# Performance work log

Hardware: AMD Instinct MI355X
Metric: run time of the kernel (lower is better)

Reference implementation:

```python
import jax, jax.numpy as jnp
import numpy as np

TOP_K = 2

def setup_inputs() -> dict:
    key = jax.random.key(0)
    ks = jax.random.split(key, 5)
    B, T, D, F, E = 4, 2048, 1024, 4096, 8
    s = 0.02
    return {
        "x": jax.random.normal(ks[0], (B, T, D), jnp.float32),
        "gate_w": jax.random.normal(ks[1], (D, E), jnp.float32) * s,
        "w1": jax.random.normal(ks[2], (E, D, F), jnp.float32) * s,
        "w3": jax.random.normal(ks[3], (E, D, F), jnp.float32) * s,
        "w2": jax.random.normal(ks[4], (E, F, D), jnp.float32) * s,
    }

def reference(x, gate_w, w1, w3, w2):
    # Router: logits -> softmax -> top-k -> renormalize (eval mode: no jitter)
    logits = jnp.einsum("btd,de->bte", x, gate_w)          # (B,T,E)
    probs = jax.nn.softmax(logits, axis=-1)
    expert_weights, expert_indices = jax.lax.top_k(probs, TOP_K)  # (B,T,K)
    expert_weights = expert_weights / expert_weights.sum(-1, keepdims=True)

    E = w1.shape[0]
    out = jnp.zeros_like(x)
    # Loop over small fixed expert count; per-token weight is 0 for non-routed
    # tokens, so dense compute + weighted sum matches the masked gather/scatter.
    for i in range(E):
        wi = jnp.where(expert_indices == i, expert_weights, 0.0).sum(-1)  # (B,T)
        h = jax.nn.silu(jnp.einsum("btd,df->btf", x, w1[i])) \
            * jnp.einsum("btd,df->btf", x, w3[i])                         # SwiGLU
        out = out + jnp.einsum("btf,fd->btd", h, w2[i]) * wi[..., None]
    return out
```

## Files before the change

### kernel.cpp

```cpp
#include <hip/hip_runtime.h>
#include <hip/hip_bf16.h>


#define NTOK 8192
#define DMODEL 1024
#define FDIM 4096
#define NEXP 8

typedef __attribute__((ext_vector_type(8))) short s8v;
typedef __attribute__((ext_vector_type(4))) float f4v;

__device__ __forceinline__ int imin(int a, int b){ return a < b ? a : b; }

__device__ __forceinline__ unsigned short f2b(float f){
  union { float f; unsigned u; } v; v.f = f;
  unsigned r = v.u + 0x7fffu + ((v.u >> 16) & 1u);
  return (unsigned short)(r >> 16);
}

__device__ __forceinline__ f4v mfma16(s8v a, s8v b, f4v c){
  return __builtin_amdgcn_mfma_f32_16x16x32_bf16(a, b, c, 0, 0, 0);
}

#define GLDS16(gp, lp) __builtin_amdgcn_global_load_lds(                      \
    (const __attribute__((address_space(1))) void*)(gp),                      \
    (__attribute__((address_space(3))) void*)(lp), 16, 0, 0)


__global__ void k_cvt(const float4* __restrict__ in, ushort4* __restrict__ out, int n4){
  int i = blockIdx.x * blockDim.x + threadIdx.x;
  int st = gridDim.x * blockDim.x;
  for(; i < n4; i += st){
    float4 v = in[i];
    ushort4 o;
    o.x = f2b(v.x); o.y = f2b(v.y); o.z = f2b(v.z); o.w = f2b(v.w);
    out[i] = o;
  }
}

__global__ void k_tr(const float* __restrict__ in, unsigned short* __restrict__ out,
                     int R, int C){
  __shared__ float tile[32][33];
  const float* src = in + (size_t)blockIdx.z * R * C;
  unsigned short* dst = out + (size_t)blockIdx.z * R * C;
  int bx = blockIdx.x * 32, by = blockIdx.y * 32;
  int tx = threadIdx.x & 31, ty = threadIdx.x >> 5;
  #pragma unroll
  for(int i = 0; i < 32; i += 8)
    tile[ty + i][tx] = src[(size_t)(by + ty + i) * C + bx + tx];
  __syncthreads();
  #pragma unroll
  for(int i = 0; i < 32; i += 8)
    dst[(size_t)(bx + ty + i) * R + by + tx] = f2b(tile[tx][ty + i]);
}

__global__ void k_router(const float* __restrict__ x, const float* __restrict__ gw,
                         int* __restrict__ route_e, float* __restrict__ route_w,
                         int* __restrict__ counts){
  int lane = threadIdx.x & 63;
  int t = blockIdx.x * 4 + (threadIdx.x >> 6);
  const float* xr = x + (size_t)t * DMODEL;
  float acc[NEXP];
  #pragma unroll
  for(int e = 0; e < NEXP; e++) acc[e] = 0.f;
  for(int d = lane; d < DMODEL; d += 64){
    float xv = xr[d];
    const float* g = gw + d * NEXP;
    #pragma unroll
    for(int e = 0; e < NEXP; e++) acc[e] += xv * g[e];
  }
  #pragma unroll
  for(int off = 32; off > 0; off >>= 1){
    #pragma unroll
    for(int e = 0; e < NEXP; e++) acc[e] += __shfl_down(acc[e], off, 64);
  }
  if(lane == 0){
    float mx = acc[0];
    #pragma unroll
    for(int e = 1; e < NEXP; e++) mx = fmaxf(mx, acc[e]);
    float p[NEXP];
    #pragma unroll
    for(int e = 0; e < NEXP; e++) p[e] = expf(acc[e] - mx);
    int i0 = 0;
    #pragma unroll
    for(int e = 1; e < NEXP; e++) if(p[e] > p[i0]) i0 = e;
    int i1 = (i0 == 0) ? 1 : 0;
    #pragma unroll
    for(int e = 0; e < NEXP; e++) if(e != i0 && p[e] > p[i1]) i1 = e;
    float inv = 1.f / (p[i0] + p[i1]);
    route_e[2*t]   = i0; route_e[2*t+1] = i1;
    route_w[2*t]   = p[i0] * inv;
    route_w[2*t+1] = p[i1] * inv;
    atomicAdd(&counts[i0], 1); atomicAdd(&counts[i1], 1);
  }
}

__global__ void k_scan(const int* __restrict__ counts, int* __restrict__ offsets,
                       int* __restrict__ cursor){
  if(threadIdx.x == 0){
    int o = 0;
    for(int e = 0; e < NEXP; e++){ offsets[e] = o; o += counts[e]; cursor[e] = 0; }
    offsets[NEXP] = o;
  }
}

__global__ void k_fill(const int* __restrict__ route_e, const float* __restrict__ route_w,
                       const int* __restrict__ offsets, int* __restrict__ cursor,
                       int* __restrict__ pair_tok, float* __restrict__ pair_wt,
                       int* __restrict__ t2p){
  int t = blockIdx.x * blockDim.x + threadIdx.x;
  if(t >= NTOK) return;
  #pragma unroll
  for(int k = 0; k < 2; k++){
    int e = route_e[2*t + k];
    int pos = atomicAdd(&cursor[e], 1);
    int gidx = offsets[e] + pos;
    pair_tok[gidx] = t;
    pair_wt[gidx] = route_w[2*t + k];
    t2p[2*t + k] = gidx;
  }
}

__global__ __launch_bounds__(256, 2) void k_ffn1(
    const unsigned short* __restrict__ xb,
    const unsigned short* __restrict__ w1t,
    const unsigned short* __restrict__ w3t,
    const int* __restrict__ counts, const int* __restrict__ offsets,
    const int* __restrict__ pair_tok,
    unsigned short* __restrict__ h)
{
  int e = blockIdx.z;
  int cnt = counts[e];
  int m0 = blockIdx.x * 128;
  if(m0 >= cnt) return;
  int off = offsets[e];
  int n0 = blockIdx.y * 128;

  __shared__ short As[2][128*32];
  __shared__ short B1s[2][128*32];
  __shared__ short B3s[2][128*32];
  __shared__ int stok[128];

  int tid = threadIdx.x;
  if(tid < 128){
    int pr = m0 + tid;
    stok[tid] = pair_tok[off + imin(pr, cnt - 1)];
  }
  __syncthreads();

  int wave = tid >> 6, lane = tid & 63;
  int rr  = wave * 32 + (lane >> 2);
  int g16 = (((lane & 3) ^ ((lane >> 3) & 3))) * 16;
  int wo = wave * 32 * 32;

  const char* a0 = (const char*)xb + (size_t)stok[rr]      * (DMODEL*2) + g16;
  const char* a1 = (const char*)xb + (size_t)stok[rr + 16] * (DMODEL*2) + g16;
  const char* b1base = (const char*)w1t + ((size_t)e * FDIM + n0) * (DMODEL*2);
  const char* b3base = (const char*)w3t + ((size_t)e * FDIM + n0) * (DMODEL*2);
  const char* b1_0 = b1base + (size_t)rr * (DMODEL*2) + g16;
  const char* b1_1 = b1_0 + (size_t)16 * (DMODEL*2);
  const char* b3_0 = b3base + (size_t)rr * (DMODEL*2) + g16;
  const char* b3_1 = b3_0 + (size_t)16 * (DMODEL*2);

  f4v zero = {0.f, 0.f, 0.f, 0.f};
  f4v acc1[4][4], acc3[4][4];
  #pragma unroll
  for(int i = 0; i < 4; i++)
    #pragma unroll
    for(int j = 0; j < 4; j++){ acc1[i][j] = zero; acc3[i][j] = zero; }

  int wm = wave & 1, wn = wave >> 1;
  int lm = lane & 15, quad = lane >> 4;
  int rp = (quad ^ ((lm >> 1) & 3)) * 8;

  GLDS16(a0,   As[0]  + wo); GLDS16(a1,   As[0]  + wo + 512);
  GLDS16(b1_0, B1s[0] + wo); GLDS16(b1_1, B1s[0] + wo + 512);
  GLDS16(b3_0, B3s[0] + wo); GLDS16(b3_1, B3s[0] + wo + 512);
  __syncthreads();

  for(int kt = 0; kt < DMODEL; kt += 32){
    int c = (kt >> 5) & 1;
    if(kt + 32 < DMODEL){
      int kb = (kt + 32) * 2;
      short* an  = As[c^1]  + wo;
      short* b1n = B1s[c^1] + wo;
      short* b3n = B3s[c^1] + wo;
      GLDS16(a0   + kb, an);  GLDS16(a1   + kb, an  + 512);
      GLDS16(b1_0 + kb, b1n); GLDS16(b1_1 + kb, b1n + 512);
      GLDS16(b3_0 + kb, b3n); GLDS16(b3_1 + kb, b3n + 512);
    }

    const short* Ab  = As[c];
    const short* B1b = B1s[c];
    const short* B3b = B3s[c];
    s8v af[4], b1f[4], b3f[4];
    #pragma unroll
    for(int mi = 0; mi < 4; mi++)
      af[mi] = *(const s8v*)(Ab + (wm*64 + mi*16 + lm)*32 + rp);
    #pragma unroll
    for(int ni = 0; ni < 4; ni++){
      b1f[ni] = *(const s8v*)(B1b + (wn*64 + ni*16 + lm)*32 + rp);
      b3f[ni] = *(const s8v*)(B3b + (wn*64 + ni*16 + lm)*32 + rp);
    }
    #pragma unroll
    for(int mi = 0; mi < 4; mi++)
      #pragma unroll
      for(int ni = 0; ni < 4; ni++){
        acc1[mi][ni] = mfma16(af[mi], b1f[ni], acc1[mi][ni]);
        acc3[mi][ni] = mfma16(af[mi], b3f[ni], acc3[mi][ni]);
      }
    __syncthreads();
  }

  #pragma unroll
  for(int mi = 0; mi < 4; mi++){
    int prb = m0 + wm*64 + mi*16 + quad*4;
    #pragma unroll
    for(int i = 0; i < 4; i++){
      int pr = prb + i;
      if(pr < cnt){
        size_t hrow = (size_t)(off + pr) * FDIM + n0 + wn*64 + lm;
        #pragma unroll
        for(int ni = 0; ni < 4; ni++){
          float p = acc1[mi][ni][i];
          float q = acc3[mi][ni][i];
          float hv = (p / (1.f + __expf(-p))) * q;
          h[hrow + ni*16] = f2b(hv);
        }
      }
    }
  }
}

__global__ __launch_bounds__(256, 2) void k_ffn2(
    const unsigned short* __restrict__ h,
    const unsigned short* __restrict__ w2t,
    const int* __restrict__ counts, const int* __restrict__ offsets,
    const float* __restrict__ pair_wt,
    float* __restrict__ pout)
{
  int e = blockIdx.z;
  int cnt = counts[e];
  int m0 = blockIdx.x * 128;
  if(m0 >= cnt) return;
  int off = offsets[e];
  int n0 = blockIdx.y * 128;

  __shared__ short As[2][128*32];
  __shared__ short Bs[2][128*32];

  int tid = threadIdx.x, wave = tid >> 6, lane = tid & 63;
  int rr  = wave * 32 + (lane >> 2);
  int g16 = (((lane & 3) ^ ((lane >> 3) & 3))) * 16;
  int wo = wave * 32 * 32;

  int pr0 = imin(m0 + rr,      cnt - 1);
  int pr1 = imin(m0 + rr + 16, cnt - 1);
  const char* a0 = (const char*)h + (size_t)(off + pr0) * (FDIM*2) + g16;
  const char* a1 = (const char*)h + (size_t)(off + pr1) * (FDIM*2) + g16;
  const char* bbase = (const char*)w2t + ((size_t)e * DMODEL + n0) * (FDIM*2);
  const char* b0 = bbase + (size_t)rr * (FDIM*2) + g16;
  const char* b1p = b0 + (size_t)16 * (FDIM*2);

  f4v zero = {0.f, 0.f, 0.f, 0.f};
  f4v acc[4][4];
  #pragma unroll
  for(int i = 0; i < 4; i++)
    #pragma unroll
    for(int j = 0; j < 4; j++) acc[i][j] = zero;

  int wm = wave & 1, wn = wave >> 1;
  int lm = lane & 15, quad = lane >> 4;
  int rp = (quad ^ ((lm >> 1) & 3)) * 8;

  GLDS16(a0, As[0] + wo); GLDS16(a1,  As[0] + wo + 512);
  GLDS16(b0, Bs[0] + wo); GLDS16(b1p, Bs[0] + wo + 512);
  __syncthreads();

  for(int kt = 0; kt < FDIM; kt += 32){
    int c = (kt >> 5) & 1;
    if(kt + 32 < FDIM){
      int kb = (kt + 32) * 2;
      short* an = As[c^1] + wo;
      short* bn = Bs[c^1] + wo;
      GLDS16(a0  + kb, an); GLDS16(a1  + kb, an + 512);
      GLDS16(b0  + kb, bn); GLDS16(b1p + kb, bn + 512);
    }

    const short* Ab = As[c];
    const short* Bb = Bs[c];
    s8v af[4], bf[4];
    #pragma unroll
    for(int mi = 0; mi < 4; mi++)
      af[mi] = *(const s8v*)(Ab + (wm*64 + mi*16 + lm)*32 + rp);
    #pragma unroll
    for(int ni = 0; ni < 4; ni++)
      bf[ni] = *(const s8v*)(Bb + (wn*64 + ni*16 + lm)*32 + rp);
    #pragma unroll
    for(int mi = 0; mi < 4; mi++)
      #pragma unroll
      for(int ni = 0; ni < 4; ni++)
        acc[mi][ni] = mfma16(af[mi], bf[ni], acc[mi][ni]);
    __syncthreads();
  }

  #pragma unroll
  for(int mi = 0; mi < 4; mi++){
    int prb = m0 + wm*64 + mi*16 + quad*4;
    #pragma unroll
    for(int i = 0; i < 4; i++){
      int pr = prb + i;
      if(pr < cnt){
        int gp = off + pr;
        float wt = pair_wt[gp];
        float* prow = pout + (size_t)gp * DMODEL + n0 + wn*64 + lm;
        #pragma unroll
        for(int ni = 0; ni < 4; ni++)
          prow[ni*16] = acc[mi][ni][i] * wt;
      }
    }
  }
}

__global__ void k_combine(const float4* __restrict__ pout, const int* __restrict__ t2p,
                          float4* __restrict__ out){
  int t = blockIdx.x;
  int d = threadIdx.x;
  int p0 = t2p[2*t], p1 = t2p[2*t + 1];
  out[(size_t)t * 256 + d] = pout[(size_t)p0 * 256 + d] + pout[(size_t)p1 * 256 + d];
}

extern "C" void kernel_launch(void* const* d_in, const int* in_sizes, int n_in,
                              void* d_out, int out_size, void* d_ws, size_t ws_size,
                              hipStream_t stream){
  const float* x  = (const float*)d_in[0];
  const float* gw = (const float*)d_in[1];
  const float* w1 = (const float*)d_in[2];
  const float* w3 = (const float*)d_in[3];
  const float* w2 = (const float*)d_in[4];
  float* out = (float*)d_out;

  char* ws = (char*)d_ws;
  size_t o = 0;
  auto alloc = [&](size_t b){ size_t r = o; o += (b + 255) & ~(size_t)255; return r; };
  unsigned short* xb  = (unsigned short*)(ws + alloc((size_t)NTOK * DMODEL * 2));
  unsigned short* w1t = (unsigned short*)(ws + alloc((size_t)NEXP * DMODEL * FDIM * 2));
  unsigned short* w3t = (unsigned short*)(ws + alloc((size_t)NEXP * DMODEL * FDIM * 2));
  unsigned short* w2t = (unsigned short*)(ws + alloc((size_t)NEXP * DMODEL * FDIM * 2));
  unsigned short* h   = (unsigned short*)(ws + alloc((size_t)2 * NTOK * FDIM * 2));
  int*   route_e  = (int*)  (ws + alloc(2 * NTOK * 4));
  float* route_w  = (float*)(ws + alloc(2 * NTOK * 4));
  int*   counts   = (int*)  (ws + alloc(256));
  int*   offsets  = (int*)  (ws + alloc(256));
  int*   cursor   = (int*)  (ws + alloc(256));
  int*   pair_tok = (int*)  (ws + alloc(2 * NTOK * 4));
  float* pair_wt  = (float*)(ws + alloc(2 * NTOK * 4));
  int*   t2p      = (int*)  (ws + alloc(2 * NTOK * 4));
  float* pout = (float*)w1t;

  hipMemsetAsync(counts, 0, 256, stream);

  k_cvt<<<2048, 256, 0, stream>>>((const float4*)x, (ushort4*)xb, NTOK * DMODEL / 4);
  k_tr<<<dim3(FDIM/32, DMODEL/32, NEXP), 256, 0, stream>>>(w1, w1t, DMODEL, FDIM);
  k_tr<<<dim3(FDIM/32, DMODEL/32, NEXP), 256, 0, stream>>>(w3, w3t, DMODEL, FDIM);
  k_tr<<<dim3(DMODEL/32, FDIM/32, NEXP), 256, 0, stream>>>(w2, w2t, FDIM, DMODEL);

  k_router<<<NTOK/4, 256, 0, stream>>>(x, gw, route_e, route_w, counts);
  k_scan<<<1, 64, 0, stream>>>(counts, offsets, cursor);
  k_fill<<<NTOK/256, 256, 0, stream>>>(route_e, route_w, offsets, cursor, pair_tok, pair_wt, t2p);

  k_ffn1<<<dim3(64, FDIM/128, NEXP), 256, 0, stream>>>(xb, w1t, w3t, counts, offsets, pair_tok, h);
  k_ffn2<<<dim3(64, DMODEL/128, NEXP), 256, 0, stream>>>(h, w2t, counts, offsets, pair_wt, pout);
  k_combine<<<NTOK, 256, 0, stream>>>((const float4*)pout, t2p, (float4*)out);
}
```

Before: 1.630 ms.

## Restructure grouped GEMMs with 512-thread tiles, split-phase pipelining and block swizzle

```diff
diff --git a/kernel.cpp b/kernel.cpp
--- a/kernel.cpp
+++ b/kernel.cpp
@@ -6,9 +6,12 @@
 #define DMODEL 1024
 #define FDIM 4096
 #define NEXP 8
+#define NT1 (DMODEL/64)
+#define NT2 (FDIM/64)
 
 typedef __attribute__((ext_vector_type(8))) short s8v;
 typedef __attribute__((ext_vector_type(4))) float f4v;
+typedef __attribute__((ext_vector_type(8))) unsigned short us8;
 
 __device__ __forceinline__ int imin(int a, int b){ return a < b ? a : b; }
 
@@ -25,6 +28,11 @@
 #define GLDS16(gp, lp) __builtin_amdgcn_global_load_lds(                      \
     (const __attribute__((address_space(1))) void*)(gp),                      \
     (__attribute__((address_space(3))) void*)(lp), 16, 0, 0)
+
+#define WAIT_LGK  asm volatile("s_waitcnt lgkmcnt(0)" ::: "memory")
+#define WAIT_V4   asm volatile("s_waitcnt vmcnt(4) lgkmcnt(0)" ::: "memory")
+#define WAIT_V0   asm volatile("s_waitcnt vmcnt(0) lgkmcnt(0)" ::: "memory")
+#define BAR       __builtin_amdgcn_s_barrier()
 
 
 __global__ void k_cvt(const float4* __restrict__ in, ushort4* __restrict__ out, int n4){
@@ -40,18 +48,28 @@
 
 __global__ void k_tr(const float* __restrict__ in, unsigned short* __restrict__ out,
                      int R, int C){
-  __shared__ float tile[32][33];
+  __shared__ float tile[64][65];
   const float* src = in + (size_t)blockIdx.z * R * C;
   unsigned short* dst = out + (size_t)blockIdx.z * R * C;
-  int bx = blockIdx.x * 32, by = blockIdx.y * 32;
-  int tx = threadIdx.x & 31, ty = threadIdx.x >> 5;
-  #pragma unroll
-  for(int i = 0; i < 32; i += 8)
-    tile[ty + i][tx] = src[(size_t)(by + ty + i) * C + bx + tx];
+  int bx = blockIdx.x * 64, by = blockIdx.y * 64;
+  int tid = threadIdx.x;
+  int tx = tid & 15, ty = tid >> 4;
+  #pragma unroll
+  for(int i = 0; i < 64; i += 16){
+    float4 v = *(const float4*)&src[(size_t)(by + ty + i) * C + bx + tx*4];
+    tile[ty + i][tx*4 + 0] = v.x; tile[ty + i][tx*4 + 1] = v.y;
+    tile[ty + i][tx*4 + 2] = v.z; tile[ty + i][tx*4 + 3] = v.w;
+  }
   __syncthreads();
-  #pragma unroll
-  for(int i = 0; i < 32; i += 8)
-    dst[(size_t)(bx + ty + i) * R + by + tx] = f2b(tile[tx][ty + i]);
+  int oc = tid & 7, orow = tid >> 3;
+  #pragma unroll
+  for(int i = 0; i < 64; i += 32){
+    int r = orow + i;
+    us8 o;
+    #pragma unroll
+    for(int j = 0; j < 8; j++) o[j] = f2b(tile[oc*8 + j][r]);
+    *(us8*)&dst[(size_t)(bx + r) * R + by + oc*8] = o;
+  }
 }
 
 __global__ void k_router(const float* __restrict__ x, const float* __restrict__ gw,
@@ -121,7 +139,7 @@
   }
 }
 
-__global__ __launch_bounds__(256, 2) void k_ffn1(
+__global__ __launch_bounds__(512, 2) void k_ffn1(
     const unsigned short* __restrict__ xb,
     const unsigned short* __restrict__ w1t,
     const unsigned short* __restrict__ w3t,
@@ -129,38 +147,48 @@
     const int* __restrict__ pair_tok,
     unsigned short* __restrict__ h)
 {
-  int e = blockIdx.z;
+  unsigned lin = blockIdx.x + ((blockIdx.y + (blockIdx.z << 5)) << 6);
+  unsigned swz = ((lin & 7u) << 11) | (lin >> 3);
+  int e  = swz >> 11;
+  int bx = swz & 63;
+  int by = (swz >> 6) & 31;
+
   int cnt = counts[e];
-  int m0 = blockIdx.x * 128;
+  int m0 = bx * 256;
   if(m0 >= cnt) return;
   int off = offsets[e];
-  int n0 = blockIdx.y * 128;
-
-  __shared__ short As[2][128*32];
-  __shared__ short B1s[2][128*32];
-  __shared__ short B3s[2][128*32];
-  __shared__ int stok[128];
+  int n0 = by * 128;
+
+  __shared__ short As[2][2][256][32];
+  __shared__ short B1s[2][2][128][32];
+  __shared__ short B3s[2][2][128][32];
+  __shared__ int stok[256];
 
   int tid = threadIdx.x;
-  if(tid < 128){
-    int pr = m0 + tid;
-    stok[tid] = pair_tok[off + imin(pr, cnt - 1)];
-  }
+  if(tid < 256) stok[tid] = pair_tok[off + imin(m0 + tid, cnt - 1)];
   __syncthreads();
 
-  int wave = tid >> 6, lane = tid & 63;
-  int rr  = wave * 32 + (lane >> 2);
-  int g16 = (((lane & 3) ^ ((lane >> 3) & 3))) * 16;
-  int wo = wave * 32 * 32;
-
-  const char* a0 = (const char*)xb + (size_t)stok[rr]      * (DMODEL*2) + g16;
-  const char* a1 = (const char*)xb + (size_t)stok[rr + 16] * (DMODEL*2) + g16;
-  const char* b1base = (const char*)w1t + ((size_t)e * FDIM + n0) * (DMODEL*2);
-  const char* b3base = (const char*)w3t + ((size_t)e * FDIM + n0) * (DMODEL*2);
-  const char* b1_0 = b1base + (size_t)rr * (DMODEL*2) + g16;
-  const char* b1_1 = b1_0 + (size_t)16 * (DMODEL*2);
-  const char* b3_0 = b3base + (size_t)rr * (DMODEL*2) + g16;
-  const char* b3_1 = b3_0 + (size_t)16 * (DMODEL*2);
+  int w = tid >> 6, lane = tid & 63;
+  int lr = lane >> 2, g = lane & 3;
+  int gs = (g ^ ((lr >> 1) & 3)) * 16;
+
+  int rA0 = w*32 + lr, rA1 = rA0 + 16;
+  int rB  = w*16 + lr;
+  const char* pA0 = (const char*)xb + (size_t)stok[rA0] * (DMODEL*2) + gs;
+  const char* pA1 = (const char*)xb + (size_t)stok[rA1] * (DMODEL*2) + gs;
+  const char* pB1 = (const char*)w1t + ((size_t)e*FDIM + n0 + rB) * (DMODEL*2) + gs;
+  const char* pB3 = (const char*)w3t + ((size_t)e*FDIM + n0 + rB) * (DMODEL*2) + gs;
+
+  auto stageA = [&](int kt, int kk, int buf){
+    int kb = kt*128 + kk*64;
+    GLDS16(pA0 + kb, &As[buf][kk][w*32][0]);
+    GLDS16(pA1 + kb, &As[buf][kk][w*32 + 16][0]);
+  };
+  auto stageB = [&](int kt, int kk, int buf){
+    int kb = kt*128 + kk*64;
+    GLDS16(pB1 + kb, &B1s[buf][kk][w*16][0]);
+    GLDS16(pB3 + kb, &B3s[buf][kk][w*16][0]);
+  };
 
   f4v zero = {0.f, 0.f, 0.f, 0.f};
   f4v acc1[4][4], acc3[4][4];
@@ -169,47 +197,92 @@
     #pragma unroll
     for(int j = 0; j < 4; j++){ acc1[i][j] = zero; acc3[i][j] = zero; }
 
-  int wm = wave & 1, wn = wave >> 1;
+  int wm = w & 3, wn = w >> 2;
   int lm = lane & 15, quad = lane >> 4;
   int rp = (quad ^ ((lm >> 1) & 3)) * 8;
 
-  GLDS16(a0,   As[0]  + wo); GLDS16(a1,   As[0]  + wo + 512);
-  GLDS16(b1_0, B1s[0] + wo); GLDS16(b1_1, B1s[0] + wo + 512);
-  GLDS16(b3_0, B3s[0] + wo); GLDS16(b3_1, B3s[0] + wo + 512);
-  __syncthreads();
-
-  for(int kt = 0; kt < DMODEL; kt += 32){
-    int c = (kt >> 5) & 1;
-    if(kt + 32 < DMODEL){
-      int kb = (kt + 32) * 2;
-      short* an  = As[c^1]  + wo;
-      short* b1n = B1s[c^1] + wo;
-      short* b3n = B3s[c^1] + wo;
-      GLDS16(a0   + kb, an);  GLDS16(a1   + kb, an  + 512);
-      GLDS16(b1_0 + kb, b1n); GLDS16(b1_1 + kb, b1n + 512);
-      GLDS16(b3_0 + kb, b3n); GLDS16(b3_1 + kb, b3n + 512);
-    }
-
-    const short* Ab  = As[c];
-    const short* B1b = B1s[c];
-    const short* B3b = B3s[c];
-    s8v af[4], b1f[4], b3f[4];
-    #pragma unroll
-    for(int mi = 0; mi < 4; mi++)
-      af[mi] = *(const s8v*)(Ab + (wm*64 + mi*16 + lm)*32 + rp);
-    #pragma unroll
-    for(int ni = 0; ni < 4; ni++){
-      b1f[ni] = *(const s8v*)(B1b + (wn*64 + ni*16 + lm)*32 + rp);
-      b3f[ni] = *(const s8v*)(B3b + (wn*64 + ni*16 + lm)*32 + rp);
-    }
-    #pragma unroll
-    for(int mi = 0; mi < 4; mi++)
+  stageA(0, 0, 0); stageB(0, 0, 0); stageA(0, 1, 0); stageB(0, 1, 0);
+  WAIT_V4; BAR;
+
+  s8v b1f[4], b3f[4];
+  for(int t = 0; t < NT1; ++t){
+    int buf = t & 1;
+    bool last = (t == NT1 - 1);
+
+    if(!last) stageA(t+1, 0, buf^1);
+    {
+      s8v a0 = *(const s8v*)&As[buf][0][wm*64 +  0 + lm][rp];
+      s8v a1 = *(const s8v*)&As[buf][0][wm*64 + 16 + lm][rp];
       #pragma unroll
       for(int ni = 0; ni < 4; ni++){
-        acc1[mi][ni] = mfma16(af[mi], b1f[ni], acc1[mi][ni]);
-        acc3[mi][ni] = mfma16(af[mi], b3f[ni], acc3[mi][ni]);
-      }
-    __syncthreads();
+        b1f[ni] = *(const s8v*)&B1s[buf][0][wn*64 + ni*16 + lm][rp];
+        b3f[ni] = *(const s8v*)&B3s[buf][0][wn*64 + ni*16 + lm][rp];
+      }
+      __builtin_amdgcn_s_setprio(1);
+      #pragma unroll
+      for(int ni = 0; ni < 4; ni++){
+        acc1[0][ni] = mfma16(a0, b1f[ni], acc1[0][ni]);
+        acc3[0][ni] = mfma16(a0, b3f[ni], acc3[0][ni]);
+        acc1[1][ni] = mfma16(a1, b1f[ni], acc1[1][ni]);
+        acc3[1][ni] = mfma16(a1, b3f[ni], acc3[1][ni]);
+      }
+      __builtin_amdgcn_s_setprio(0);
+    }
+    WAIT_LGK; BAR;
+
+    if(!last) stageB(t+1, 0, buf^1);
+    {
+      s8v a2 = *(const s8v*)&As[buf][0][wm*64 + 32 + lm][rp];
+      s8v a3 = *(const s8v*)&As[buf][0][wm*64 + 48 + lm][rp];
+      __builtin_amdgcn_s_setprio(1);
+      #pragma unroll
+      for(int ni = 0; ni < 4; ni++){
+        acc1[2][ni] = mfma16(a2, b1f[ni], acc1[2][ni]);
+        acc3[2][ni] = mfma16(a2, b3f[ni], acc3[2][ni]);
+        acc1[3][ni] = mfma16(a3, b1f[ni], acc1[3][ni]);
+        acc3[3][ni] = mfma16(a3, b3f[ni], acc3[3][ni]);
+      }
+      __builtin_amdgcn_s_setprio(0);
+    }
+    if(!last) WAIT_V4; else WAIT_V0;
+    BAR;
+
+    if(!last) stageA(t+1, 1, buf^1);
+    {
+      s8v a0 = *(const s8v*)&As[buf][1][wm*64 +  0 + lm][rp];
+      s8v a1 = *(const s8v*)&As[buf][1][wm*64 + 16 + lm][rp];
+      #pragma unroll
+      for(int ni = 0; ni < 4; ni++){
+        b1f[ni] = *(const s8v*)&B1s[buf][1][wn*64 + ni*16 + lm][rp];
+        b3f[ni] = *(const s8v*)&B3s[buf][1][wn*64 + ni*16 + lm][rp];
+      }
+      __builtin_amdgcn_s_setprio(1);
+      #pragma unroll
+      for(int ni = 0; ni < 4; ni++){
+        acc1[0][ni] = mfma16(a0, b1f[ni], acc1[0][ni]);
+        acc3[0][ni] = mfma16(a0, b3f[ni], acc3[0][ni]);
+        acc1[1][ni] = mfma16(a1, b1f[ni], acc1[1][ni]);
+        acc3[1][ni] = mfma16(a1, b3f[ni], acc3[1][ni]);
+      }
+      __builtin_amdgcn_s_setprio(0);
+    }
+    WAIT_LGK; BAR;
+
+    if(!last) stageB(t+1, 1, buf^1);
+    {
+      s8v a2 = *(const s8v*)&As[buf][1][wm*64 + 32 + lm][rp];
+      s8v a3 = *(const s8v*)&As[buf][1][wm*64 + 48 + lm][rp];
+      __builtin_amdgcn_s_setprio(1);
+      #pragma unroll
+      for(int ni = 0; ni < 4; ni++){
+        acc1[2][ni] = mfma16(a2, b1f[ni], acc1[2][ni]);
+        acc3[2][ni] = mfma16(a2, b3f[ni], acc3[2][ni]);
+        acc1[3][ni] = mfma16(a3, b1f[ni], acc1[3][ni]);
+        acc3[3][ni] = mfma16(a3, b3f[ni], acc3[3][ni]);
+      }
+      __builtin_amdgcn_s_setprio(0);
+    }
+    if(!last){ WAIT_V4; BAR; }
   }
 
   #pragma unroll
@@ -225,88 +298,151 @@
           float p = acc1[mi][ni][i];
           float q = acc3[mi][ni][i];
           float hv = (p / (1.f + __expf(-p))) * q;
-          h[hrow + ni*16] = f2b(hv);
+          __builtin_nontemporal_store((unsigned short)f2b(hv), &h[hrow + ni*16]);
         }
       }
     }
   }
 }
 
-__global__ __launch_bounds__(256, 2) void k_ffn2(
+__global__ __launch_bounds__(512, 2) void k_ffn2(
     const unsigned short* __restrict__ h,
     const unsigned short* __restrict__ w2t,
     const int* __restrict__ counts, const int* __restrict__ offsets,
     const float* __restrict__ pair_wt,
     float* __restrict__ pout)
 {
-  int e = blockIdx.z;
+  unsigned lin = blockIdx.x + ((blockIdx.y + (blockIdx.z << 2)) << 6);
+  unsigned swz = ((lin & 7u) << 8) | (lin >> 3);
+  int e  = swz >> 8;
+  int bx = swz & 63;
+  int by = (swz >> 6) & 3;
+
   int cnt = counts[e];
-  int m0 = blockIdx.x * 128;
+  int m0 = bx * 256;
   if(m0 >= cnt) return;
   int off = offsets[e];
-  int n0 = blockIdx.y * 128;
-
-  __shared__ short As[2][128*32];
-  __shared__ short Bs[2][128*32];
-
-  int tid = threadIdx.x, wave = tid >> 6, lane = tid & 63;
-  int rr  = wave * 32 + (lane >> 2);
-  int g16 = (((lane & 3) ^ ((lane >> 3) & 3))) * 16;
-  int wo = wave * 32 * 32;
-
-  int pr0 = imin(m0 + rr,      cnt - 1);
-  int pr1 = imin(m0 + rr + 16, cnt - 1);
-  const char* a0 = (const char*)h + (size_t)(off + pr0) * (FDIM*2) + g16;
-  const char* a1 = (const char*)h + (size_t)(off + pr1) * (FDIM*2) + g16;
-  const char* bbase = (const char*)w2t + ((size_t)e * DMODEL + n0) * (FDIM*2);
-  const char* b0 = bbase + (size_t)rr * (FDIM*2) + g16;
-  const char* b1p = b0 + (size_t)16 * (FDIM*2);
+  int n0 = by * 256;
+
+  __shared__ short As[2][2][256][32];
+  __shared__ short Bs[2][2][256][32];
+
+  int tid = threadIdx.x, w = tid >> 6, lane = tid & 63;
+  int lr = lane >> 2, g = lane & 3;
+  int gs = (g ^ ((lr >> 1) & 3)) * 16;
+
+  int rA0 = w*32 + lr, rA1 = rA0 + 16;
+  int pr0 = imin(m0 + rA0, cnt - 1), pr1 = imin(m0 + rA1, cnt - 1);
+  const char* pA0 = (const char*)h + (size_t)(off + pr0) * (FDIM*2) + gs;
+  const char* pA1 = (const char*)h + (size_t)(off + pr1) * (FDIM*2) + gs;
+  const char* pB0 = (const char*)w2t + ((size_t)e*DMODEL + n0 + rA0) * (FDIM*2) + gs;
+  const char* pB1 = (const char*)w2t + ((size_t)e*DMODEL + n0 + rA1) * (FDIM*2) + gs;
+
+  auto stageA = [&](int kt, int kk, int buf){
+    int kb = kt*128 + kk*64;
+    GLDS16(pA0 + kb, &As[buf][kk][w*32][0]);
+    GLDS16(pA1 + kb, &As[buf][kk][w*32 + 16][0]);
+  };
+  auto stageB = [&](int kt, int kk, int buf){
+    int kb = kt*128 + kk*64;
+    GLDS16(pB0 + kb, &Bs[buf][kk][w*32][0]);
+    GLDS16(pB1 + kb, &Bs[buf][kk][w*32 + 16][0]);
+  };
 
   f4v zero = {0.f, 0.f, 0.f, 0.f};
-  f4v acc[4][4];
-  #pragma unroll
-  for(int i = 0; i < 4; i++)
+  f4v acc[8][4];
+  #pragma unroll
+  for(int i = 0; i < 8; i++)
     #pragma unroll
     for(int j = 0; j < 4; j++) acc[i][j] = zero;
 
-  int wm = wave & 1, wn = wave >> 1;
+  int wm = w & 1, wn = w >> 1;
   int lm = lane & 15, quad = lane >> 4;
   int rp = (quad ^ ((lm >> 1) & 3)) * 8;
 
-  GLDS16(a0, As[0] + wo); GLDS16(a1,  As[0] + wo + 512);
-  GLDS16(b0, Bs[0] + wo); GLDS16(b1p, Bs[0] + wo + 512);
-  __syncthreads();
-
-  for(int kt = 0; kt < FDIM; kt += 32){
-    int c = (kt >> 5) & 1;
-    if(kt + 32 < FDIM){
-      int kb = (kt + 32) * 2;
-      short* an = As[c^1] + wo;
-      short* bn = Bs[c^1] + wo;
-      GLDS16(a0  + kb, an); GLDS16(a1  + kb, an + 512);
-      GLDS16(b0  + kb, bn); GLDS16(b1p + kb, bn + 512);
-    }
-
-    const short* Ab = As[c];
-    const short* Bb = Bs[c];
-    s8v af[4], bf[4];
-    #pragma unroll
-    for(int mi = 0; mi < 4; mi++)
-      af[mi] = *(const s8v*)(Ab + (wm*64 + mi*16 + lm)*32 + rp);
-    #pragma unroll
-    for(int ni = 0; ni < 4; ni++)
-      bf[ni] = *(const s8v*)(Bb + (wn*64 + ni*16 + lm)*32 + rp);
-    #pragma unroll
-    for(int mi = 0; mi < 4; mi++)
+  stageA(0, 0, 0); stageB(0, 0, 0); stageA(0, 1, 0); stageB(0, 1, 0);
+  WAIT_V4; BAR;
+
+  s8v bf[4];
+  for(int t = 0; t < NT2; ++t){
+    int buf = t & 1;
+    bool last = (t == NT2 - 1);
+
+    if(!last) stageA(t+1, 0, buf^1);
+    {
+      s8v af[4];
+      #pragma unroll
+      for(int mi = 0; mi < 4; mi++)
+        af[mi] = *(const s8v*)&As[buf][0][wm*128 + mi*16 + lm][rp];
       #pragma unroll
       for(int ni = 0; ni < 4; ni++)
-        acc[mi][ni] = mfma16(af[mi], bf[ni], acc[mi][ni]);
-    __syncthreads();
-  }
-
-  #pragma unroll
-  for(int mi = 0; mi < 4; mi++){
-    int prb = m0 + wm*64 + mi*16 + quad*4;
+        bf[ni] = *(const s8v*)&Bs[buf][0][wn*64 + ni*16 + lm][rp];
+      __builtin_amdgcn_s_setprio(1);
+      #pragma unroll
+      for(int mi = 0; mi < 4; mi++)
+        #pragma unroll
+        for(int ni = 0; ni < 4; ni++)
+          acc[mi][ni] = mfma16(af[mi], bf[ni], acc[mi][ni]);
+      __builtin_amdgcn_s_setprio(0);
+    }
+    WAIT_LGK; BAR;
+
+    if(!last) stageB(t+1, 0, buf^1);
+    {
+      s8v af[4];
+      #pragma unroll
+      for(int mi = 0; mi < 4; mi++)
+        af[mi] = *(const s8v*)&As[buf][0][wm*128 + (4+mi)*16 + lm][rp];
+      __builtin_amdgcn_s_setprio(1);
+      #pragma unroll
+      for(int mi = 0; mi < 4; mi++)
+        #pragma unroll
+        for(int ni = 0; ni < 4; ni++)
+          acc[4+mi][ni] = mfma16(af[mi], bf[ni], acc[4+mi][ni]);
+      __builtin_amdgcn_s_setprio(0);
+    }
+    if(!last) WAIT_V4; else WAIT_V0;
+    BAR;
+
+    if(!last) stageA(t+1, 1, buf^1);
+    {
+      s8v af[4];
+      #pragma unroll
+      for(int mi = 0; mi < 4; mi++)
+        af[mi] = *(const s8v*)&As[buf][1][wm*128 + mi*16 + lm][rp];
+      #pragma unroll
+      for(int ni = 0; ni < 4; ni++)
+        bf[ni] = *(const s8v*)&Bs[buf][1][wn*64 + ni*16 + lm][rp];
+      __builtin_amdgcn_s_setprio(1);
+      #pragma unroll
+      for(int mi = 0; mi < 4; mi++)
+        #pragma unroll
+        for(int ni = 0; ni < 4; ni++)
+          acc[mi][ni] = mfma16(af[mi], bf[ni], acc[mi][ni]);
+      __builtin_amdgcn_s_setprio(0);
+    }
+    WAIT_LGK; BAR;
+
+    if(!last) stageB(t+1, 1, buf^1);
+    {
+      s8v af[4];
+      #pragma unroll
+      for(int mi = 0; mi < 4; mi++)
+        af[mi] = *(const s8v*)&As[buf][1][wm*128 + (4+mi)*16 + lm][rp];
+      __builtin_amdgcn_s_setprio(1);
+      #pragma unroll
+      for(int mi = 0; mi < 4; mi++)
+        #pragma unroll
+        for(int ni = 0; ni < 4; ni++)
+          acc[4+mi][ni] = mfma16(af[mi], bf[ni], acc[4+mi][ni]);
+      __builtin_amdgcn_s_setprio(0);
+    }
+    if(!last){ WAIT_V4; BAR; }
+  }
+
+  #pragma unroll
+  for(int mi = 0; mi < 8; mi++){
+    int prb = m0 + wm*128 + mi*16 + quad*4;
     #pragma unroll
     for(int i = 0; i < 4; i++){
       int pr = prb + i;
@@ -316,7 +452,7 @@
         float* prow = pout + (size_t)gp * DMODEL + n0 + wn*64 + lm;
         #pragma unroll
         for(int ni = 0; ni < 4; ni++)
-          prow[ni*16] = acc[mi][ni][i] * wt;
+          __builtin_nontemporal_store(acc[mi][ni][i] * wt, prow + ni*16);
       }
     }
   }
@@ -361,15 +497,15 @@
   hipMemsetAsync(counts, 0, 256, stream);
 
   k_cvt<<<2048, 256, 0, stream>>>((const float4*)x, (ushort4*)xb, NTOK * DMODEL / 4);
-  k_tr<<<dim3(FDIM/32, DMODEL/32, NEXP), 256, 0, stream>>>(w1, w1t, DMODEL, FDIM);
-  k_tr<<<dim3(FDIM/32, DMODEL/32, NEXP), 256, 0, stream>>>(w3, w3t, DMODEL, FDIM);
-  k_tr<<<dim3(DMODEL/32, FDIM/32, NEXP), 256, 0, stream>>>(w2, w2t, FDIM, DMODEL);
+  k_tr<<<dim3(FDIM/64, DMODEL/64, NEXP), 256, 0, stream>>>(w1, w1t, DMODEL, FDIM);
+  k_tr<<<dim3(FDIM/64, DMODEL/64, NEXP), 256, 0, stream>>>(w3, w3t, DMODEL, FDIM);
+  k_tr<<<dim3(DMODEL/64, FDIM/64, NEXP), 256, 0, stream>>>(w2, w2t, FDIM, DMODEL);
 
   k_router<<<NTOK/4, 256, 0, stream>>>(x, gw, route_e, route_w, counts);
   k_scan<<<1, 64, 0, stream>>>(counts, offsets, cursor);
   k_fill<<<NTOK/256, 256, 0, stream>>>(route_e, route_w, offsets, cursor, pair_tok, pair_wt, t2p);
 
-  k_ffn1<<<dim3(64, FDIM/128, NEXP), 256, 0, stream>>>(xb, w1t, w3t, counts, offsets, pair_tok, h);
-  k_ffn2<<<dim3(64, DMODEL/128, NEXP), 256, 0, stream>>>(h, w2t, counts, offsets, pair_wt, pout);
+  k_ffn1<<<dim3(64, FDIM/128, NEXP), 512, 0, stream>>>(xb, w1t, w3t, counts, offsets, pair_tok, h);
+  k_ffn2<<<dim3(64, DMODEL/256, NEXP), 512, 0, stream>>>(h, w2t, counts, offsets, pair_wt, pout);
   k_combine<<<NTOK, 256, 0, stream>>>((const float4*)pout, t2p, (float4*)out);
 }
```

After: 1.486 ms. 1.1x faster.
